# Kernel optimization log

Hardware: AMD Instinct MI355X
Metric: run time of the kernel (lower is better)

The kernel has to match this reference:

```python
import jax, jax.numpy as jnp
import numpy as np
from jax import lax

SEQ, BATCH, INPUT, HIDDEN = 2048, 32, 256, 256


def setup_inputs() -> dict:
    key = jax.random.key(0)
    k1, k2, k3 = jax.random.split(key, 3)
    scale = 1.0 / np.sqrt(HIDDEN)
    return {
        "input": jax.random.normal(k1, (SEQ, BATCH, INPUT), dtype=jnp.float32),
        "W_ih": jax.random.normal(k2, (3 * HIDDEN, INPUT), dtype=jnp.float32) * scale,
        "W_hh": jax.random.normal(k3, (3 * HIDDEN, HIDDEN), dtype=jnp.float32) * scale,
        "b_ih": jnp.zeros((3 * HIDDEN,), dtype=jnp.float32),
        "b_hh": jnp.zeros((3 * HIDDEN,), dtype=jnp.float32),
    }


def reference(input, W_ih, W_hh, b_ih, b_hh):
    """Single-layer unidirectional CustomGRU forward.

    Faithful to the torch module, including its quirk: the n-gate gets the
    W_hh_n @ h contribution twice (once un-gated via `gates`, once gated by r).
    Returns (output [S,B,H], h_n [1,B,H]).
    """
    H = W_hh.shape[0] // 3
    W_hn = W_hh[2 * H:]  # [H, H]
    # Precompute input projections for all timesteps (same math, batched GEMM).
    x_proj = jnp.einsum('sbi,gi->sbg', input, W_ih) + b_ih + b_hh  # [S,B,3H]

    def step(h, xp):
        gates = xp + h @ W_hh.T  # [B, 3H]
        r, z, n = jnp.split(gates, 3, axis=1)
        r = jax.nn.sigmoid(r)
        z = jax.nn.sigmoid(z)
        n = jnp.tanh(n + r * (h @ W_hn.T))
        h_new = (1.0 - z) * n + z * h
        return h_new, h_new

    h0 = jnp.zeros((input.shape[1], H), dtype=input.dtype)
    h_last, output = lax.scan(step, h0, x_proj)
    return output, h_last[None, :, :]
```

## Files before the change

kernel.cpp:

```cpp
#include <hip/hip_runtime.h>
#include <stdint.h>
#include <stddef.h>

#define S_LEN 2048
#define BATCH 32
#define NIN   256
#define NH    256
#define NG    768

typedef _Float16 half2_t __attribute__((ext_vector_type(2)));
typedef _Float16 half8_t __attribute__((ext_vector_type(8)));
typedef int      int16v  __attribute__((ext_vector_type(16)));

#if __has_builtin(__builtin_amdgcn_exp2f)
#define EXP2F(x) __builtin_amdgcn_exp2f(x)
#else
#define EXP2F(x) exp2f(x)
#endif

static __device__ __forceinline__ float fdot2(half2_t a, half2_t b, float c) {
  return __builtin_amdgcn_fdot2(a, b, c, false);
}
static __device__ __forceinline__ half2_t pack2(float lo, float hi) {
  half2_t r; r[0] = (_Float16)lo; r[1] = (_Float16)hi; return r;
}
static __device__ __forceinline__ float sigmoid_fast(float x) {
  float e = EXP2F(-1.44269504088896340736f * x);
  return 1.0f / (1.0f + e);
}
static __device__ __forceinline__ float tanh_fast(float x) {
  float e = EXP2F(2.88539008177792681472f * x);
  return 1.0f - 2.0f / (1.0f + e);
}

#define BH(x)    __builtin_bit_cast(half2_t, (x))
#define BW(W, e) __builtin_bit_cast(half2_t, (int)((W)[e]))

#define DOT16(W, i0) do {                                                     \
    int4 q0 = hls[(i0) + 0], q1 = hls[(i0) + 1];                              \
    int4 q2 = hls[(i0) + 2], q3 = hls[(i0) + 3];                              \
    a0 = fdot2(BH(q0.x), BW(W, 0),  a0); a1 = fdot2(BH(q0.y), BW(W, 1),  a1);\
    a2 = fdot2(BH(q0.z), BW(W, 2),  a2); a3 = fdot2(BH(q0.w), BW(W, 3),  a3);\
    a0 = fdot2(BH(q1.x), BW(W, 4),  a0); a1 = fdot2(BH(q1.y), BW(W, 5),  a1);\
    a2 = fdot2(BH(q1.z), BW(W, 6),  a2); a3 = fdot2(BH(q1.w), BW(W, 7),  a3);\
    a0 = fdot2(BH(q2.x), BW(W, 8),  a0); a1 = fdot2(BH(q2.y), BW(W, 9),  a1);\
    a2 = fdot2(BH(q2.z), BW(W, 10), a2); a3 = fdot2(BH(q2.w), BW(W, 11), a3);\
    a0 = fdot2(BH(q3.x), BW(W, 12), a0); a1 = fdot2(BH(q3.y), BW(W, 13), a1);\
    a2 = fdot2(BH(q3.z), BW(W, 14), a2); a3 = fdot2(BH(q3.w), BW(W, 15), a3);\
  } while (0)

#define LDW(W, o) do {                                                        \
    int4 q0 = wsrc[(o) + 0], q1 = wsrc[(o) + 1];                              \
    int4 q2 = wsrc[(o) + 2], q3 = wsrc[(o) + 3];                              \
    W = (int16v){q0.x, q0.y, q0.z, q0.w, q1.x, q1.y, q1.z, q1.w,              \
                 q2.x, q2.y, q2.z, q2.w, q3.x, q3.y, q3.z, q3.w};             \
  } while (0)

__global__ __launch_bounds__(256) void prep_in_kernel(const float* __restrict__ in,
                                                      _Float16* __restrict__ in16) {
  size_t v = (size_t)blockIdx.x * 256 + threadIdx.x;
  const float4* p4 = (const float4*)in;
  float4 a = p4[v * 2 + 0];
  float4 b = p4[v * 2 + 1];
  half8_t o;
  o[0] = (_Float16)a.x; o[1] = (_Float16)a.y; o[2] = (_Float16)a.z; o[3] = (_Float16)a.w;
  o[4] = (_Float16)b.x; o[5] = (_Float16)b.y; o[6] = (_Float16)b.z; o[7] = (_Float16)b.w;
  ((half8_t*)in16)[v] = o;
}

__global__ __launch_bounds__(256) void prep_w_kernel(const float* __restrict__ W_ih,
                                                     const float* __restrict__ W_hh,
                                                     const float* __restrict__ b_ih,
                                                     const float* __restrict__ b_hh,
                                                     half2_t* __restrict__ whh2g,
                                                     half2_t* __restrict__ wih2,
                                                     float* __restrict__ bias) {
  int idx = blockIdx.x * 256 + threadIdx.x;
  if (idx < 128 * NG) {
    int g = idx >> 7, kk = idx & 127;
    whh2g[idx] = pack2(W_hh[(size_t)g * NH + 2 * kk], W_hh[(size_t)g * NH + 2 * kk + 1]);
  } else if (idx < 2 * 128 * NG) {
    int i2 = idx - 128 * NG;
    int g = i2 >> 7, kk = i2 & 127;
    wih2[(size_t)g * 128 + kk] = pack2(W_ih[(size_t)g * NIN + 2 * kk], W_ih[(size_t)g * NIN + 2 * kk + 1]);
  } else if (idx < 2 * 128 * NG + NG) {
    int g = idx - 2 * 128 * NG;
    bias[g] = b_ih[g] + b_hh[g];
  }
}

__global__
__attribute__((amdgpu_flat_work_group_size(768, 768), amdgpu_waves_per_eu(3, 3)))
void xproj_kernel(const _Float16* __restrict__ in16,
                  const half2_t* __restrict__ wih2,
                  const float* __restrict__ bias,
                  float* __restrict__ xp_out) {
  __shared__ char occ_pad[86016];
  {
    unsigned lp = (unsigned)(uintptr_t)&occ_pad[0];
    asm volatile("" :: "v"(lp));
  }
  const int g = threadIdx.x;
  const int row0 = blockIdx.x * 64;
  const float bg = bias[g];

  int16v w0, w1, w2, w3, w4, w5, w6, w7;
  {
    const int4* wsrc = (const int4*)(wih2 + (size_t)g * 128);
    LDW(w0, 0);  LDW(w1, 4);  LDW(w2, 8);  LDW(w3, 12);
    LDW(w4, 16); LDW(w5, 20); LDW(w6, 24); LDW(w7, 28);
  }

  for (int r = 0; r < 64; ++r) {
    const int row = row0 + r;
    const int4* hls = (const int4*)(in16 + (size_t)row * NIN);
    float a0 = 0.f, a1 = 0.f, a2 = 0.f, a3 = 0.f;
    DOT16(w0, 0);  DOT16(w1, 4);  DOT16(w2, 8);  DOT16(w3, 12);
    DOT16(w4, 16); DOT16(w5, 20); DOT16(w6, 24); DOT16(w7, 28);
    xp_out[(size_t)row * NG + g] = (a0 + a1) + (a2 + a3) + bg;
  }
}

struct SMemG {
  int   hbuf_i[2][128];
  float mv[NG];
  char  pad[81920];
};
static_assert(sizeof(SMemG) == 86016, "LDS clamp size");

__global__
__attribute__((amdgpu_flat_work_group_size(768, 768), amdgpu_waves_per_eu(3, 3)))
void gru_kernel(const float* __restrict__ xp,
                const half2_t* __restrict__ whh2g,
                float* __restrict__ out) {
  const int b = blockIdx.x;
  const int g = threadIdx.x;

  int16v w0, w1, w2, w3, w4, w5, w6, w7;
  {
    const int4* wsrc = (const int4*)(whh2g + (size_t)g * 128);
    LDW(w0, 0);  LDW(w1, 4);  LDW(w2, 8);  LDW(w3, 12);
    LDW(w4, 16); LDW(w5, 20); LDW(w6, 24); LDW(w7, 28);
  }

  __shared__ SMemG sm;
  {
    unsigned lp = (unsigned)(uintptr_t)&sm.pad[0];
    asm volatile("" :: "v"(lp));
  }

  if (g < NH) ((_Float16*)sm.hbuf_i)[g] = (_Float16)0.f;

  const float* xq = xp + (size_t)b * NG + g;
  float xr_c = 0.f, xz_c = 0.f, xn_c = 0.f;
  if (g < NH) { xr_c = xq[0]; xz_c = xq[NH]; xn_c = xq[2 * NH]; }
  xq += (size_t)BATCH * NG;
  float* op = out + (size_t)b * NH + g;

  float h = 0.f;
  __syncthreads();

  for (int t = 0; t < S_LEN; ++t) {
    float xr_n = 0.f, xz_n = 0.f, xn_n = 0.f;
    if (g < NH) { xr_n = xq[0]; xz_n = xq[NH]; xn_n = xq[2 * NH]; }

    const int4* hls = ((const int4*)sm.hbuf_i) + ((t & 1) << 5);
    float a0 = 0.f, a1 = 0.f, a2 = 0.f, a3 = 0.f;
    DOT16(w0, 0);  DOT16(w1, 4);  DOT16(w2, 8);  DOT16(w3, 12);
    DOT16(w4, 16); DOT16(w5, 20); DOT16(w6, 24); DOT16(w7, 28);
    sm.mv[g] = (a0 + a1) + (a2 + a3);
    __syncthreads();

    if (g < NH) {
      float mvr = sm.mv[g], mvz = sm.mv[NH + g], mvn = sm.mv[2 * NH + g];
      float r = sigmoid_fast(xr_c + mvr);
      float z = sigmoid_fast(xz_c + mvz);
      float n = tanh_fast(xn_c + mvn + r * mvn);
      h = z * (h - n) + n;
      op[0] = h;
      ((_Float16*)sm.hbuf_i)[(((t + 1) & 1) << 8) + g] = (_Float16)h;
    }
    __syncthreads();

    xr_c = xr_n; xz_c = xz_n; xn_c = xn_n;
    xq += (size_t)BATCH * NG;
    op += (size_t)BATCH * NH;
  }

  if (g < NH) out[(size_t)S_LEN * BATCH * NH + (size_t)b * NH + g] = h;
}

extern "C" void kernel_launch(void* const* d_in, const int* in_sizes, int n_in,
                              void* d_out, int out_size, void* d_ws, size_t ws_size,
                              hipStream_t stream) {
  const float* input = (const float*)d_in[0];
  const float* W_ih  = (const float*)d_in[1];
  const float* W_hh  = (const float*)d_in[2];
  const float* b_ih  = (const float*)d_in[3];
  const float* b_hh  = (const float*)d_in[4];
  float* out = (float*)d_out;

  const size_t SB = (size_t)S_LEN * BATCH;
  const size_t xp_b   = SB * NG * 4;
  const size_t in16_b = SB * NIN * 2;
  const size_t w_b    = (size_t)128 * NG * 4;

  char* p = (char*)d_ws;
  float*    xp    = (float*)p;                p += xp_b;
  _Float16* in16  = (_Float16*)p;             p += in16_b;
  half2_t*  whh2g = (half2_t*)p;              p += w_b;
  half2_t*  wih2  = (half2_t*)p;              p += w_b;
  float*    bias  = (float*)p;

  prep_in_kernel<<<8192, 256, 0, stream>>>(input, in16);
  prep_w_kernel<<<(2 * 128 * NG + NG + 255) / 256, 256, 0, stream>>>(W_ih, W_hh, b_ih, b_hh,
                                                                     whh2g, wih2, bias);
  xproj_kernel<<<1024, 768, 0, stream>>>(in16, wih2, bias, xp);
  gru_kernel<<<BATCH, 768, 0, stream>>>(xp, whh2g, out);
  (void)out_size; (void)n_in; (void)in_sizes; (void)ws_size;
}
```

Before: 2.796 ms.

## Broadcast hidden state through scalar loads from global instead of LDS

```diff
diff --git a/kernel.cpp b/kernel.cpp
--- a/kernel.cpp
+++ b/kernel.cpp
@@ -49,12 +49,29 @@
     a2 = fdot2(BH(q3.z), BW(W, 14), a2); a3 = fdot2(BH(q3.w), BW(W, 15), a3);\
   } while (0)
 
+#define DOTS(HS, W) do {                                                      \
+    a0 = fdot2(BW(HS, 0),  BW(W, 0),  a0); a1 = fdot2(BW(HS, 1),  BW(W, 1),  a1);\
+    a2 = fdot2(BW(HS, 2),  BW(W, 2),  a2); a3 = fdot2(BW(HS, 3),  BW(W, 3),  a3);\
+    a0 = fdot2(BW(HS, 4),  BW(W, 4),  a0); a1 = fdot2(BW(HS, 5),  BW(W, 5),  a1);\
+    a2 = fdot2(BW(HS, 6),  BW(W, 6),  a2); a3 = fdot2(BW(HS, 7),  BW(W, 7),  a3);\
+    a0 = fdot2(BW(HS, 8),  BW(W, 8),  a0); a1 = fdot2(BW(HS, 9),  BW(W, 9),  a1);\
+    a2 = fdot2(BW(HS, 10), BW(W, 10), a2); a3 = fdot2(BW(HS, 11), BW(W, 11), a3);\
+    a0 = fdot2(BW(HS, 12), BW(W, 12), a0); a1 = fdot2(BW(HS, 13), BW(W, 13), a1);\
+    a2 = fdot2(BW(HS, 14), BW(W, 14), a2); a3 = fdot2(BW(HS, 15), BW(W, 15), a3);\
+  } while (0)
+
 #define LDW(W, o) do {                                                        \
     int4 q0 = wsrc[(o) + 0], q1 = wsrc[(o) + 1];                              \
     int4 q2 = wsrc[(o) + 2], q3 = wsrc[(o) + 3];                              \
     W = (int16v){q0.x, q0.y, q0.z, q0.w, q1.x, q1.y, q1.z, q1.w,              \
                  q2.x, q2.y, q2.z, q2.w, q3.x, q3.y, q3.z, q3.w};             \
   } while (0)
+
+#define SLOAD(dst, base, off) \
+  asm volatile("s_load_dwordx16 %0, %1, " off : "=s"(dst) : "s"(base))
+#define SWAIT1(a)       asm volatile("s_waitcnt lgkmcnt(0)" : "+s"(a))
+#define SWAIT2(a, b)    asm volatile("s_waitcnt lgkmcnt(0)" : "+s"(a), "+s"(b))
+#define SWAIT3(a, b, c) asm volatile("s_waitcnt lgkmcnt(0)" : "+s"(a), "+s"(b), "+s"(c))
 
 __global__ __launch_bounds__(256) void prep_in_kernel(const float* __restrict__ in,
                                                       _Float16* __restrict__ in16) {
@@ -122,9 +139,8 @@
 }
 
 struct SMemG {
-  int   hbuf_i[2][128];
   float mv[NG];
-  char  pad[81920];
+  char  pad[86016 - NG * 4];
 };
 static_assert(sizeof(SMemG) == 86016, "LDS clamp size");
 
@@ -132,6 +148,7 @@
 __attribute__((amdgpu_flat_work_group_size(768, 768), amdgpu_waves_per_eu(3, 3)))
 void gru_kernel(const float* __restrict__ xp,
                 const half2_t* __restrict__ whh2g,
+                _Float16* __restrict__ hglob,
                 float* __restrict__ out) {
   const int b = blockIdx.x;
   const int g = threadIdx.x;
@@ -149,7 +166,10 @@
     asm volatile("" :: "v"(lp));
   }
 
-  if (g < NH) ((_Float16*)sm.hbuf_i)[g] = (_Float16)0.f;
+  _Float16* hsb = hglob + ((size_t)b << 9);
+  const uint64_t hbase = (uint64_t)(uintptr_t)hsb;
+
+  if (g < 128) ((int*)hsb)[g] = 0;
 
   const float* xq = xp + (size_t)b * NG + g;
   float xr_c = 0.f, xz_c = 0.f, xn_c = 0.f;
@@ -161,13 +181,28 @@
   __syncthreads();
 
   for (int t = 0; t < S_LEN; ++t) {
+    asm volatile("s_dcache_inv" ::: "memory");
+
     float xr_n = 0.f, xz_n = 0.f, xn_n = 0.f;
     if (g < NH) { xr_n = xq[0]; xz_n = xq[NH]; xn_n = xq[2 * NH]; }
 
-    const int4* hls = ((const int4*)sm.hbuf_i) + ((t & 1) << 5);
+    const uint64_t hb = hbase | (uint64_t)((t & 1) << 9);
+    int16v s0, s1, s2, s3, s4, s5, s6, s7;
     float a0 = 0.f, a1 = 0.f, a2 = 0.f, a3 = 0.f;
-    DOT16(w0, 0);  DOT16(w1, 4);  DOT16(w2, 8);  DOT16(w3, 12);
-    DOT16(w4, 16); DOT16(w5, 20); DOT16(w6, 24); DOT16(w7, 28);
+
+    SLOAD(s0, hb, "0x0"); SLOAD(s1, hb, "0x40"); SLOAD(s2, hb, "0x80");
+    SWAIT3(s0, s1, s2);
+    SLOAD(s3, hb, "0xc0"); SLOAD(s4, hb, "0x100");
+    DOTS(s0, w0); DOTS(s1, w1); DOTS(s2, w2);
+    SWAIT2(s3, s4);
+    SLOAD(s5, hb, "0x140"); SLOAD(s6, hb, "0x180");
+    DOTS(s3, w3); DOTS(s4, w4);
+    SWAIT2(s5, s6);
+    SLOAD(s7, hb, "0x1c0");
+    DOTS(s5, w5); DOTS(s6, w6);
+    SWAIT1(s7);
+    DOTS(s7, w7);
+
     sm.mv[g] = (a0 + a1) + (a2 + a3);
     __syncthreads();
 
@@ -178,7 +213,7 @@
       float n = tanh_fast(xn_c + mvn + r * mvn);
       h = z * (h - n) + n;
       op[0] = h;
-      ((_Float16*)sm.hbuf_i)[(((t + 1) & 1) << 8) + g] = (_Float16)h;
+      hsb[(((t + 1) & 1) << 8) + g] = (_Float16)h;
     }
     __syncthreads();
 
@@ -210,12 +245,14 @@
   _Float16* in16  = (_Float16*)p;             p += in16_b;
   half2_t*  whh2g = (half2_t*)p;              p += w_b;
   half2_t*  wih2  = (half2_t*)p;              p += w_b;
-  float*    bias  = (float*)p;
+  float*    bias  = (float*)p;                p += (size_t)NG * 4;
+  uintptr_t hp = (((uintptr_t)p) + 1023) & ~(uintptr_t)1023;
+  _Float16* hglob = (_Float16*)hp;
 
   prep_in_kernel<<<8192, 256, 0, stream>>>(input, in16);
   prep_w_kernel<<<(2 * 128 * NG + NG + 255) / 256, 256, 0, stream>>>(W_ih, W_hh, b_ih, b_hh,
                                                                      whh2g, wih2, bias);
   xproj_kernel<<<1024, 768, 0, stream>>>(in16, wih2, bias, xp);
-  gru_kernel<<<BATCH, 768, 0, stream>>>(xp, whh2g, out);
+  gru_kernel<<<BATCH, 768, 0, stream>>>(xp, whh2g, hglob, out);
   (void)out_size; (void)n_in; (void)in_sizes; (void)ws_size;
 }
```

Result: no change. 2.827 ms (+1.1%).

## Split each hidden unit's three gate dot-products across a thread pair with DPP reduction

Applied to the files above, without the earlier changes.

```diff
diff --git a/kernel.cpp b/kernel.cpp
--- a/kernel.cpp
+++ b/kernel.cpp
@@ -31,6 +31,11 @@
 static __device__ __forceinline__ float tanh_fast(float x) {
   float e = EXP2F(2.88539008177792681472f * x);
   return 1.0f - 2.0f / (1.0f + e);
+}
+
+static __device__ __forceinline__ float pair_sum(float v) {
+  int y = __builtin_amdgcn_mov_dpp(__builtin_bit_cast(int, v), 0xB1, 0xF, 0xF, true);
+  return v + __builtin_bit_cast(float, y);
 }
 
 #define BH(x)    __builtin_bit_cast(half2_t, (x))
@@ -49,6 +54,25 @@
     a2 = fdot2(BH(q3.z), BW(W, 14), a2); a3 = fdot2(BH(q3.w), BW(W, 15), a3);\
   } while (0)
 
+#define DOT24(q0, q1, WR, WZ, WN, o) do {                                               \
+  ar0 = fdot2(BH(q0.x), BW(WR,(o)+0), ar0); az0 = fdot2(BH(q0.x), BW(WZ,(o)+0), az0);  \
+  an0 = fdot2(BH(q0.x), BW(WN,(o)+0), an0);                                            \
+  ar1 = fdot2(BH(q0.y), BW(WR,(o)+1), ar1); az1 = fdot2(BH(q0.y), BW(WZ,(o)+1), az1);  \
+  an1 = fdot2(BH(q0.y), BW(WN,(o)+1), an1);                                            \
+  ar0 = fdot2(BH(q0.z), BW(WR,(o)+2), ar0); az0 = fdot2(BH(q0.z), BW(WZ,(o)+2), az0);  \
+  an0 = fdot2(BH(q0.z), BW(WN,(o)+2), an0);                                            \
+  ar1 = fdot2(BH(q0.w), BW(WR,(o)+3), ar1); az1 = fdot2(BH(q0.w), BW(WZ,(o)+3), az1);  \
+  an1 = fdot2(BH(q0.w), BW(WN,(o)+3), an1);                                            \
+  ar0 = fdot2(BH(q1.x), BW(WR,(o)+4), ar0); az0 = fdot2(BH(q1.x), BW(WZ,(o)+4), az0);  \
+  an0 = fdot2(BH(q1.x), BW(WN,(o)+4), an0);                                            \
+  ar1 = fdot2(BH(q1.y), BW(WR,(o)+5), ar1); az1 = fdot2(BH(q1.y), BW(WZ,(o)+5), az1);  \
+  an1 = fdot2(BH(q1.y), BW(WN,(o)+5), an1);                                            \
+  ar0 = fdot2(BH(q1.z), BW(WR,(o)+6), ar0); az0 = fdot2(BH(q1.z), BW(WZ,(o)+6), az0);  \
+  an0 = fdot2(BH(q1.z), BW(WN,(o)+6), an0);                                            \
+  ar1 = fdot2(BH(q1.w), BW(WR,(o)+7), ar1); az1 = fdot2(BH(q1.w), BW(WZ,(o)+7), az1);  \
+  an1 = fdot2(BH(q1.w), BW(WN,(o)+7), an1);                                            \
+} while (0)
+
 #define LDW(W, o) do {                                                        \
     int4 q0 = wsrc[(o) + 0], q1 = wsrc[(o) + 1];                              \
     int4 q2 = wsrc[(o) + 2], q3 = wsrc[(o) + 3];                              \
@@ -72,13 +96,20 @@
                                                      const float* __restrict__ W_hh,
                                                      const float* __restrict__ b_ih,
                                                      const float* __restrict__ b_hh,
-                                                     half2_t* __restrict__ whh2g,
+                                                     half2_t* __restrict__ whh3,
                                                      half2_t* __restrict__ wih2,
                                                      float* __restrict__ bias) {
   int idx = blockIdx.x * 256 + threadIdx.x;
   if (idx < 128 * NG) {
-    int g = idx >> 7, kk = idx & 127;
-    whh2g[idx] = pack2(W_hh[(size_t)g * NH + 2 * kk], W_hh[(size_t)g * NH + 2 * kk + 1]);
+    int kk = idx & 63;
+    int r1 = idx >> 6;
+    int gate = r1 % 3;
+    int r2 = r1 / 3;
+    int cc = r2 & 1;
+    int jj = r2 >> 1;
+    int row = gate * NH + jj;
+    int col = cc * 128 + 2 * kk;
+    whh3[idx] = pack2(W_hh[(size_t)row * NH + col], W_hh[(size_t)row * NH + col + 1]);
   } else if (idx < 2 * 128 * NG) {
     int i2 = idx - 128 * NG;
     int g = i2 >> 7, kk = i2 & 127;
@@ -121,73 +152,81 @@
   }
 }
 
-struct SMemG {
-  int   hbuf_i[2][128];
-  float mv[NG];
-  char  pad[81920];
-};
-static_assert(sizeof(SMemG) == 86016, "LDS clamp size");
-
 __global__
-__attribute__((amdgpu_flat_work_group_size(768, 768), amdgpu_waves_per_eu(3, 3)))
+__attribute__((amdgpu_flat_work_group_size(512, 512), amdgpu_waves_per_eu(2, 2)))
 void gru_kernel(const float* __restrict__ xp,
-                const half2_t* __restrict__ whh2g,
+                const half2_t* __restrict__ whh3,
                 float* __restrict__ out) {
-  const int b = blockIdx.x;
-  const int g = threadIdx.x;
-
-  int16v w0, w1, w2, w3, w4, w5, w6, w7;
+  const int b   = blockIdx.x;
+  const int tid = threadIdx.x;
+  const int j   = tid >> 1;
+  const int c   = tid & 1;
+
+  int16v wr0, wr1, wr2, wr3, wz0, wz1, wz2, wz3, wn0, wn1, wn2, wn3;
   {
-    const int4* wsrc = (const int4*)(whh2g + (size_t)g * 128);
-    LDW(w0, 0);  LDW(w1, 4);  LDW(w2, 8);  LDW(w3, 12);
-    LDW(w4, 16); LDW(w5, 20); LDW(w6, 24); LDW(w7, 28);
-  }
-
-  __shared__ SMemG sm;
-  {
-    unsigned lp = (unsigned)(uintptr_t)&sm.pad[0];
-    asm volatile("" :: "v"(lp));
-  }
-
-  if (g < NH) ((_Float16*)sm.hbuf_i)[g] = (_Float16)0.f;
-
-  const float* xq = xp + (size_t)b * NG + g;
-  float xr_c = 0.f, xz_c = 0.f, xn_c = 0.f;
-  if (g < NH) { xr_c = xq[0]; xz_c = xq[NH]; xn_c = xq[2 * NH]; }
+    const int4* wsrc = (const int4*)(whh3 + (size_t)tid * 192);
+    LDW(wr0, 0);  LDW(wr1, 4);  LDW(wr2, 8);  LDW(wr3, 12);
+    LDW(wz0, 16); LDW(wz1, 20); LDW(wz2, 24); LDW(wz3, 28);
+    LDW(wn0, 32); LDW(wn1, 36); LDW(wn2, 40); LDW(wn3, 44);
+  }
+
+  __shared__ __attribute__((aligned(16))) char smh[1088];
+  if (tid < 272) ((int*)smh)[tid] = 0;
+
+  const float* xq = xp + (size_t)b * NG + j;
+  float xr_c = xq[0], xz_c = xq[NH], xn_c = xq[2 * NH];
   xq += (size_t)BATCH * NG;
-  float* op = out + (size_t)b * NH + g;
+  float* op = out + (size_t)b * NH + j;
+
+  const int wofs = (j >> 7) * 272 + (j & 127) * 2;
 
   float h = 0.f;
   __syncthreads();
 
   for (int t = 0; t < S_LEN; ++t) {
-    float xr_n = 0.f, xz_n = 0.f, xn_n = 0.f;
-    if (g < NH) { xr_n = xq[0]; xz_n = xq[NH]; xn_n = xq[2 * NH]; }
-
-    const int4* hls = ((const int4*)sm.hbuf_i) + ((t & 1) << 5);
-    float a0 = 0.f, a1 = 0.f, a2 = 0.f, a3 = 0.f;
-    DOT16(w0, 0);  DOT16(w1, 4);  DOT16(w2, 8);  DOT16(w3, 12);
-    DOT16(w4, 16); DOT16(w5, 20); DOT16(w6, 24); DOT16(w7, 28);
-    sm.mv[g] = (a0 + a1) + (a2 + a3);
-    __syncthreads();
-
-    if (g < NH) {
-      float mvr = sm.mv[g], mvz = sm.mv[NH + g], mvn = sm.mv[2 * NH + g];
-      float r = sigmoid_fast(xr_c + mvr);
-      float z = sigmoid_fast(xz_c + mvz);
-      float n = tanh_fast(xn_c + mvn + r * mvn);
-      h = z * (h - n) + n;
+    float xr_n = xq[0], xz_n = xq[NH], xn_n = xq[2 * NH];
+
+    const char* hb = smh + (t & 1) * 544 + c * 272;
+    float ar0 = 0.f, ar1 = 0.f, az0 = 0.f, az1 = 0.f, an0 = 0.f, an1 = 0.f;
+    int4 q0, q1;
+    q0 = *(const int4*)(hb +   0); q1 = *(const int4*)(hb +  16);
+    DOT24(q0, q1, wr0, wz0, wn0, 0);
+    q0 = *(const int4*)(hb +  32); q1 = *(const int4*)(hb +  48);
+    DOT24(q0, q1, wr0, wz0, wn0, 8);
+    q0 = *(const int4*)(hb +  64); q1 = *(const int4*)(hb +  80);
+    DOT24(q0, q1, wr1, wz1, wn1, 0);
+    q0 = *(const int4*)(hb +  96); q1 = *(const int4*)(hb + 112);
+    DOT24(q0, q1, wr1, wz1, wn1, 8);
+    q0 = *(const int4*)(hb + 128); q1 = *(const int4*)(hb + 144);
+    DOT24(q0, q1, wr2, wz2, wn2, 0);
+    q0 = *(const int4*)(hb + 160); q1 = *(const int4*)(hb + 176);
+    DOT24(q0, q1, wr2, wz2, wn2, 8);
+    q0 = *(const int4*)(hb + 192); q1 = *(const int4*)(hb + 208);
+    DOT24(q0, q1, wr3, wz3, wn3, 0);
+    q0 = *(const int4*)(hb + 224); q1 = *(const int4*)(hb + 240);
+    DOT24(q0, q1, wr3, wz3, wn3, 8);
+
+    float mvr = pair_sum(ar0 + ar1);
+    float mvz = pair_sum(az0 + az1);
+    float mvn = pair_sum(an0 + an1);
+
+    float r = sigmoid_fast(xr_c + mvr);
+    float z = sigmoid_fast(xz_c + mvz);
+    float n = tanh_fast(xn_c + mvn + r * mvn);
+    h = z * (h - n) + n;
+
+    if (c == 0) {
       op[0] = h;
-      ((_Float16*)sm.hbuf_i)[(((t + 1) & 1) << 8) + g] = (_Float16)h;
+      *(_Float16*)(smh + (((t + 1) & 1) * 544) + wofs) = (_Float16)h;
     }
-    __syncthreads();
+    asm volatile("s_waitcnt lgkmcnt(0)\n\ts_barrier" ::: "memory");
 
     xr_c = xr_n; xz_c = xz_n; xn_c = xn_n;
     xq += (size_t)BATCH * NG;
     op += (size_t)BATCH * NH;
   }
 
-  if (g < NH) out[(size_t)S_LEN * BATCH * NH + (size_t)b * NH + g] = h;
+  if (c == 0) out[(size_t)S_LEN * BATCH * NH + (size_t)b * NH + j] = h;
 }
 
 extern "C" void kernel_launch(void* const* d_in, const int* in_sizes, int n_in,
@@ -208,14 +247,14 @@
   char* p = (char*)d_ws;
   float*    xp    = (float*)p;                p += xp_b;
   _Float16* in16  = (_Float16*)p;             p += in16_b;
-  half2_t*  whh2g = (half2_t*)p;              p += w_b;
+  half2_t*  whh3  = (half2_t*)p;              p += w_b;
   half2_t*  wih2  = (half2_t*)p;              p += w_b;
   float*    bias  = (float*)p;
 
   prep_in_kernel<<<8192, 256, 0, stream>>>(input, in16);
   prep_w_kernel<<<(2 * 128 * NG + NG + 255) / 256, 256, 0, stream>>>(W_ih, W_hh, b_ih, b_hh,
-                                                                     whh2g, wih2, bias);
+                                                                     whh3, wih2, bias);
   xproj_kernel<<<1024, 768, 0, stream>>>(in16, wih2, bias, xp);
-  gru_kernel<<<BATCH, 768, 0, stream>>>(xp, whh2g, out);
+  gru_kernel<<<BATCH, 512, 0, stream>>>(xp, whh3, out);
   (void)out_size; (void)n_in; (void)in_sizes; (void)ws_size;
 }
```

After: 2.679 ms. 1.04x faster.

## Use MFMA for the recurrent matvec with 16 batch rows per block

Applied to the files above, without the earlier changes.

```diff
diff --git a/kernel.cpp b/kernel.cpp
--- a/kernel.cpp
+++ b/kernel.cpp
@@ -11,6 +11,9 @@
 typedef _Float16 half2_t __attribute__((ext_vector_type(2)));
 typedef _Float16 half8_t __attribute__((ext_vector_type(8)));
 typedef int      int16v  __attribute__((ext_vector_type(16)));
+typedef _Float16 f16x8   __attribute__((ext_vector_type(8)));
+typedef _Float16 f16x4   __attribute__((ext_vector_type(4)));
+typedef float    f32x4   __attribute__((ext_vector_type(4)));
 
 #if __has_builtin(__builtin_amdgcn_exp2f)
 #define EXP2F(x) __builtin_amdgcn_exp2f(x)
@@ -31,6 +34,9 @@
 static __device__ __forceinline__ float tanh_fast(float x) {
   float e = EXP2F(2.88539008177792681472f * x);
   return 1.0f - 2.0f / (1.0f + e);
+}
+static __device__ __forceinline__ f32x4 MFMA16(f16x8 a, f16x8 b, f32x4 c) {
+  return __builtin_amdgcn_mfma_f32_16x16x32_f16(a, b, c, 0, 0, 0);
 }
 
 #define BH(x)    __builtin_bit_cast(half2_t, (x))
@@ -72,13 +78,22 @@
                                                      const float* __restrict__ W_hh,
                                                      const float* __restrict__ b_ih,
                                                      const float* __restrict__ b_hh,
-                                                     half2_t* __restrict__ whh2g,
+                                                     half2_t* __restrict__ whh4,
                                                      half2_t* __restrict__ wih2,
                                                      float* __restrict__ bias) {
   int idx = blockIdx.x * 256 + threadIdx.x;
   if (idx < 128 * NG) {
-    int g = idx >> 7, kk = idx & 127;
-    whh2g[idx] = pack2(W_hh[(size_t)g * NH + 2 * kk], W_hh[(size_t)g * NH + 2 * kk + 1]);
+    int v  = idx & 3;
+    int l  = (idx >> 2) & 63;
+    int kt = (idx >> 8) & 7;
+    int r1 = idx >> 11;
+    int gate = r1 % 3;
+    int r2 = r1 / 3;
+    int u  = r2 & 1;
+    int ww = r2 >> 1;
+    int row = gate * NH + 32 * ww + 16 * u + (l & 15);
+    int col = 32 * kt + 8 * (l >> 4) + 2 * v;
+    whh4[idx] = pack2(W_hh[(size_t)row * NH + col], W_hh[(size_t)row * NH + col + 1]);
   } else if (idx < 2 * 128 * NG) {
     int i2 = idx - 128 * NG;
     int g = i2 >> 7, kk = i2 & 127;
@@ -121,73 +136,110 @@
   }
 }
 
-struct SMemG {
-  int   hbuf_i[2][128];
-  float mv[NG];
-  char  pad[81920];
-};
-static_assert(sizeof(SMemG) == 86016, "LDS clamp size");
-
 __global__
-__attribute__((amdgpu_flat_work_group_size(768, 768), amdgpu_waves_per_eu(3, 3)))
+__attribute__((amdgpu_flat_work_group_size(512, 512), amdgpu_waves_per_eu(2, 2)))
 void gru_kernel(const float* __restrict__ xp,
-                const half2_t* __restrict__ whh2g,
+                const f16x8* __restrict__ whh4,
                 float* __restrict__ out) {
-  const int b = blockIdx.x;
-  const int g = threadIdx.x;
-
-  int16v w0, w1, w2, w3, w4, w5, w6, w7;
+  const int blk = blockIdx.x;
+  const int tid = threadIdx.x;
+  const int w   = tid >> 6;
+  const int l   = tid & 63;
+  const int lb  = l & 15;
+  const int lq  = l >> 4;
+  const int jb  = 32 * w;
+
+  f16x8 W[2][3][8];
   {
-    const int4* wsrc = (const int4*)(whh2g + (size_t)g * 128);
-    LDW(w0, 0);  LDW(w1, 4);  LDW(w2, 8);  LDW(w3, 12);
-    LDW(w4, 16); LDW(w5, 20); LDW(w6, 24); LDW(w7, 28);
-  }
-
-  __shared__ SMemG sm;
-  {
-    unsigned lp = (unsigned)(uintptr_t)&sm.pad[0];
-    asm volatile("" :: "v"(lp));
-  }
-
-  if (g < NH) ((_Float16*)sm.hbuf_i)[g] = (_Float16)0.f;
-
-  const float* xq = xp + (size_t)b * NG + g;
-  float xr_c = 0.f, xz_c = 0.f, xn_c = 0.f;
-  if (g < NH) { xr_c = xq[0]; xz_c = xq[NH]; xn_c = xq[2 * NH]; }
-  xq += (size_t)BATCH * NG;
-  float* op = out + (size_t)b * NH + g;
-
-  float h = 0.f;
+    const f16x8* wp = whh4 + (size_t)w * 3072 + l;
+#pragma unroll
+    for (int u = 0; u < 2; ++u)
+#pragma unroll
+      for (int gt = 0; gt < 3; ++gt)
+#pragma unroll
+        for (int kt = 0; kt < 8; ++kt)
+          W[u][gt][kt] = wp[(size_t)(((u * 3 + gt) * 8) + kt) * 64];
+  }
+
+  __shared__ _Float16 hbuf[2][16][264];
+  for (int i = tid; i < 16 * 264; i += 512) ((_Float16*)hbuf)[i] = (_Float16)0.f;
+
+  const float* xpl = xp  + ((size_t)blk * 16 + lb) * NG + jb + 4 * lq;
+  float*       opl = out + ((size_t)blk * 16 + lb) * NH + jb + 4 * lq;
+
+  f32x4 accR0 = *(const f32x4*)(xpl + 0 * NH +  0);
+  f32x4 accR1 = *(const f32x4*)(xpl + 0 * NH + 16);
+  f32x4 accZ0 = *(const f32x4*)(xpl + 1 * NH +  0);
+  f32x4 accZ1 = *(const f32x4*)(xpl + 1 * NH + 16);
+  f32x4 xn0   = *(const f32x4*)(xpl + 2 * NH +  0);
+  f32x4 xn1   = *(const f32x4*)(xpl + 2 * NH + 16);
+  f32x4 accN0, accN1;
+
+  float ho[2][4];
+#pragma unroll
+  for (int u = 0; u < 2; ++u)
+#pragma unroll
+    for (int q = 0; q < 4; ++q) ho[u][q] = 0.f;
+
   __syncthreads();
 
   for (int t = 0; t < S_LEN; ++t) {
-    float xr_n = 0.f, xz_n = 0.f, xn_n = 0.f;
-    if (g < NH) { xr_n = xq[0]; xz_n = xq[NH]; xn_n = xq[2 * NH]; }
-
-    const int4* hls = ((const int4*)sm.hbuf_i) + ((t & 1) << 5);
-    float a0 = 0.f, a1 = 0.f, a2 = 0.f, a3 = 0.f;
-    DOT16(w0, 0);  DOT16(w1, 4);  DOT16(w2, 8);  DOT16(w3, 12);
-    DOT16(w4, 16); DOT16(w5, 20); DOT16(w6, 24); DOT16(w7, 28);
-    sm.mv[g] = (a0 + a1) + (a2 + a3);
-    __syncthreads();
-
-    if (g < NH) {
-      float mvr = sm.mv[g], mvz = sm.mv[NH + g], mvn = sm.mv[2 * NH + g];
-      float r = sigmoid_fast(xr_c + mvr);
-      float z = sigmoid_fast(xz_c + mvz);
-      float n = tanh_fast(xn_c + mvn + r * mvn);
-      h = z * (h - n) + n;
-      op[0] = h;
-      ((_Float16*)sm.hbuf_i)[(((t + 1) & 1) << 8) + g] = (_Float16)h;
+    const _Float16* hb = &hbuf[t & 1][0][0];
+    accN0 = (f32x4){0.f, 0.f, 0.f, 0.f};
+    accN1 = (f32x4){0.f, 0.f, 0.f, 0.f};
+
+    f16x8 Ba = *(const f16x8*)(hb + lb * 264 + 8 * lq);
+#pragma unroll
+    for (int kt = 0; kt < 8; ++kt) {
+      f16x8 Bn = Ba;
+      if (kt < 7) Bn = *(const f16x8*)(hb + lb * 264 + 32 * (kt + 1) + 8 * lq);
+      accN0 = MFMA16(W[0][2][kt], Ba, accN0);
+      accN1 = MFMA16(W[1][2][kt], Ba, accN1);
+      accR0 = MFMA16(W[0][0][kt], Ba, accR0);
+      accR1 = MFMA16(W[1][0][kt], Ba, accR1);
+      accZ0 = MFMA16(W[0][1][kt], Ba, accZ0);
+      accZ1 = MFMA16(W[1][1][kt], Ba, accZ1);
+      Ba = Bn;
     }
-    __syncthreads();
-
-    xr_c = xr_n; xz_c = xz_n; xn_c = xn_n;
-    xq += (size_t)BATCH * NG;
-    op += (size_t)BATCH * NH;
-  }
-
-  if (g < NH) out[(size_t)S_LEN * BATCH * NH + (size_t)b * NH + g] = h;
+
+#define ELEM(AR, AZ, AN, XN, U) do {                                   \
+      _Pragma("unroll")                                                \
+      for (int q = 0; q < 4; ++q) {                                    \
+        float r = sigmoid_fast(AR[q]);                                 \
+        float z = sigmoid_fast(AZ[q]);                                 \
+        float mvn = AN[q];                                             \
+        float n = tanh_fast(XN[q] + mvn + r * mvn);   \
+        ho[U][q] = z * (ho[U][q] - n) + n;                             \
+      }                                                                \
+    } while (0)
+    ELEM(accR0, accZ0, accN0, xn0, 0);
+    ELEM(accR1, accZ1, accN1, xn1, 1);
+#undef ELEM
+
+    float* os = opl + (size_t)t * BATCH * NH;
+    *(f32x4*)(os +  0) = (f32x4){ho[0][0], ho[0][1], ho[0][2], ho[0][3]};
+    *(f32x4*)(os + 16) = (f32x4){ho[1][0], ho[1][1], ho[1][2], ho[1][3]};
+
+    _Float16* hw = &hbuf[(t + 1) & 1][0][0] + lb * 264 + jb + 4 * lq;
+    *(f16x4*)(hw +  0) = (f16x4){(_Float16)ho[0][0], (_Float16)ho[0][1],
+                                 (_Float16)ho[0][2], (_Float16)ho[0][3]};
+    *(f16x4*)(hw + 16) = (f16x4){(_Float16)ho[1][0], (_Float16)ho[1][1],
+                                 (_Float16)ho[1][2], (_Float16)ho[1][3]};
+
+    const float* xnp = xpl + (size_t)(t + 1) * BATCH * NG;
+    accR0 = *(const f32x4*)(xnp + 0 * NH +  0);
+    accR1 = *(const f32x4*)(xnp + 0 * NH + 16);
+    accZ0 = *(const f32x4*)(xnp + 1 * NH +  0);
+    accZ1 = *(const f32x4*)(xnp + 1 * NH + 16);
+    xn0   = *(const f32x4*)(xnp + 2 * NH +  0);
+    xn1   = *(const f32x4*)(xnp + 2 * NH + 16);
+
+    asm volatile("s_waitcnt lgkmcnt(0)\n\ts_barrier" ::: "memory");
+  }
+
+  float* fs = out + (size_t)S_LEN * BATCH * NH + ((size_t)blk * 16 + lb) * NH + jb + 4 * lq;
+  *(f32x4*)(fs +  0) = (f32x4){ho[0][0], ho[0][1], ho[0][2], ho[0][3]};
+  *(f32x4*)(fs + 16) = (f32x4){ho[1][0], ho[1][1], ho[1][2], ho[1][3]};
 }
 
 extern "C" void kernel_launch(void* const* d_in, const int* in_sizes, int n_in,
@@ -208,14 +260,14 @@
   char* p = (char*)d_ws;
   float*    xp    = (float*)p;                p += xp_b;
   _Float16* in16  = (_Float16*)p;             p += in16_b;
-  half2_t*  whh2g = (half2_t*)p;              p += w_b;
+  half2_t*  whh4  = (half2_t*)p;              p += w_b;
   half2_t*  wih2  = (half2_t*)p;              p += w_b;
   float*    bias  = (float*)p;
 
   prep_in_kernel<<<8192, 256, 0, stream>>>(input, in16);
   prep_w_kernel<<<(2 * 128 * NG + NG + 255) / 256, 256, 0, stream>>>(W_ih, W_hh, b_ih, b_hh,
-                                                                     whh2g, wih2, bias);
+                                                                     whh4, wih2, bias);
   xproj_kernel<<<1024, 768, 0, stream>>>(in16, wih2, bias, xp);
-  gru_kernel<<<BATCH, 768, 0, stream>>>(xp, whh2g, out);
+  gru_kernel<<<2, 512, 0, stream>>>(xp, (const f16x8*)whh4, out);
   (void)out_size; (void)n_in; (void)in_sizes; (void)ws_size;
 }
```

Result: slower. 5.461 ms (+95.3%).
